# Optimization experiments

Measured on AMD Instinct MI355X. Metric: run time of the kernel, lower is better.

## Reference

```python
import jax, jax.numpy as jnp
import numpy as np

B, NA, NL, D = 512, 128, 512, 128
KA, KL = 16, 16  # active_agents, lane_tokens


def _layernorm(x, g, b, eps=1e-5):
    m = x.mean(-1, keepdims=True)
    v = ((x - m) ** 2).mean(-1, keepdims=True)
    return (x - m) / jnp.sqrt(v + eps) * g + b


def setup_inputs() -> dict:
    key = jax.random.key(0)
    ks = jax.random.split(key, 16)
    s = D ** -0.5
    inp = {
        "actor_feat": jax.random.normal(ks[0], (B, NA, D), jnp.float32),
        "lane_feat": jax.random.normal(ks[1], (B, NL, D), jnp.float32),
        "lane_centers": jax.random.normal(ks[2], (B, NL, 2), jnp.float32) * 50.0,
        "x_centers": jax.random.normal(ks[3], (B, NA, 2), jnp.float32) * 50.0,
        "spike_rate": jax.random.uniform(ks[4], (B, NA), jnp.float32),
        "actor_valid": jax.random.randint(ks[5], (B, NA), 0, 2).astype(bool),
        "lane_valid": jax.random.randint(ks[6], (B, NL), 0, 2).astype(bool),
        # MLP layer 0
        "W0a": jax.random.normal(ks[7], (D, D), jnp.float32) * s,
        "b0a": jnp.zeros((D,), jnp.float32),
        "W0b": jax.random.normal(ks[8], (D, D), jnp.float32) * s,
        "b0b": jnp.zeros((D,), jnp.float32),
        # MLP layer 1
        "W1a": jax.random.normal(ks[9], (D, D), jnp.float32) * s,
        "b1a": jnp.zeros((D,), jnp.float32),
        "W1b": jax.random.normal(ks[10], (D, D), jnp.float32) * s,
        "b1b": jnp.zeros((D,), jnp.float32),
        # shared LayerNorm
        "gamma": jnp.ones((D,), jnp.float32),
        "beta": jnp.zeros((D,), jnp.float32),
    }
    return inp


def reference(actor_feat, lane_feat, lane_centers, x_centers, spike_rate,
              actor_valid, lane_valid,
              W0a, b0a, W0b, b0b, W1a, b1a, W1b, b1b, gamma, beta):
    bsel = jnp.arange(B)[:, None]  # [B,1] batch index for fancy gather/scatter

    # masked top-k over spike_rate -> active agent indices [B,KA]
    masked = jnp.where(actor_valid, spike_rate, -jnp.inf)
    _, aidx = jax.lax.top_k(masked, KA)

    # lane selection: min distance from any active agent, k smallest
    ac = x_centers[bsel, aidx]                                # [B,KA,2]
    diff = ac[:, :, None, :] - lane_centers[:, None, :, :]    # [B,KA,NL,2]
    pair_dist = jnp.sqrt((diff ** 2).sum(-1))                 # cdist [B,KA,NL]
    lane_dist = pair_dist.min(axis=1)                         # [B,NL]
    lane_dist = jnp.where(lane_valid, lane_dist, jnp.inf)
    _, lidx = jax.lax.top_k(-lane_dist, KL)                   # k smallest

    # gather nodes and run residual MLP + LayerNorm stack
    nodes = jnp.concatenate([actor_feat[bsel, aidx], lane_feat[bsel, lidx]], axis=1)  # [B,KA+KL,D]
    for (Wa, ba, Wb, bb) in ((W0a, b0a, W0b, b0b), (W1a, b1a, W1b, b1b)):
        h = jax.nn.gelu(nodes @ Wa + ba, approximate=False) @ Wb + bb
        nodes = _layernorm(nodes + h, gamma, beta)

    # scatter updated nodes back into the full pools
    actor_out = actor_feat.at[bsel, aidx].set(nodes[:, :KA])
    lane_out = lane_feat.at[bsel, lidx].set(nodes[:, KA:])
    return actor_out, lane_out
```

## Files before the change

kernel.cpp:

```cpp
#include <hip/hip_runtime.h>
#include <math.h>

#define Bsz 512
#define NA  128
#define NL  512
#define Dd  128
#define KA  16
#define KL  16

#define NIDX  512
#define NCB   3584
#define ACT4  2097152
#define TOT4  10485760
#define CSTRIDE (NCB * 256)

__global__ __launch_bounds__(256) void idx_copy_kernel(
    const float* __restrict__ spike, const unsigned char* __restrict__ avalid,
    const float* __restrict__ xc, const float* __restrict__ lc,
    const unsigned char* __restrict__ lvalid,
    const float* __restrict__ actor_feat, const float* __restrict__ lane_feat,
    int* __restrict__ aidx, int* __restrict__ lidx,
    float* __restrict__ out0, float* __restrict__ out1) {
  const int tid = threadIdx.x;

  if (blockIdx.x >= NIDX) {
    const float4* __restrict__ srcA = (const float4*)actor_feat;
    const float4* __restrict__ srcL = (const float4*)lane_feat;
    float4* __restrict__ dstA = (float4*)out0;
    float4* __restrict__ dstL = (float4*)out1;
    const int gid = (blockIdx.x - NIDX) * 256 + tid;
#pragma unroll 1
    for (int base = gid; base < TOT4; base += 4 * CSTRIDE) {
      float4 v[4]; int pp[4];
#pragma unroll
      for (int u = 0; u < 4; ++u) {
        pp[u] = base + u * CSTRIDE;
        if (pp[u] < TOT4)
          v[u] = (pp[u] < ACT4) ? srcA[pp[u]] : srcL[pp[u] - ACT4];
      }
#pragma unroll
      for (int u = 0; u < 4; ++u) {
        if (pp[u] < TOT4) {
          if (pp[u] < ACT4) dstA[pp[u]] = v[u];
          else              dstL[pp[u] - ACT4] = v[u];
        }
      }
    }
    return;
  }

  const int b = blockIdx.x;

  __shared__ float s_ax[KA], s_ay[KA];
  __shared__ int   s_ai[KA];
  __shared__ float s_ld[NL];
  __shared__ float s_rv[4];
  __shared__ int   s_ri[4];
  __shared__ int   s_flag;

  if (tid == 0) s_flag = 0;
  __syncthreads();
  {
    int any = 0;
    for (int i = tid; i < 4096; i += 256)
      if ((i & 3) && avalid[i]) any = 1;
    if (any) atomicOr(&s_flag, 1);
  }
  __syncthreads();
  const int isbyte = s_flag;

#define VALID_AT(P, I) (isbyte ? (int)(P)[I] : ((const int*)(P))[I])

  if (tid < 64) {
    float v0 = VALID_AT(avalid, b * NA + tid)      ? spike[b * NA + tid]      : -INFINITY;
    float v1 = VALID_AT(avalid, b * NA + tid + 64) ? spike[b * NA + tid + 64] : -INFINITY;
    for (int it = 0; it < KA; ++it) {
      float bv = v0; int bi = tid;
      if (v1 > bv) { bv = v1; bi = tid + 64; }
      for (int off = 32; off; off >>= 1) {
        float ov = __shfl_xor(bv, off);
        int   oi = __shfl_xor(bi, off);
        if (ov > bv || (ov == bv && oi < bi)) { bv = ov; bi = oi; }
      }
      if (bi == tid)      v0 = -INFINITY;
      if (bi == tid + 64) v1 = -INFINITY;
      if (tid == 0) s_ai[it] = bi;
    }
  }
  __syncthreads();
  if (tid < KA) {
    int a = s_ai[tid];
    aidx[b * KA + tid] = a;
    s_ax[tid] = xc[(b * NA + a) * 2 + 0];
    s_ay[tid] = xc[(b * NA + a) * 2 + 1];
  }
  __syncthreads();

  for (int l = tid; l < NL; l += 256) {
    float lx = lc[(b * NL + l) * 2 + 0];
    float ly = lc[(b * NL + l) * 2 + 1];
    float best = INFINITY;
#pragma unroll
    for (int a = 0; a < KA; ++a) {
      float dx = s_ax[a] - lx, dy = s_ay[a] - ly;
      float d2 = __fadd_rn(__fmul_rn(dx, dx), __fmul_rn(dy, dy));
      best = fminf(best, d2);
    }
    best = sqrtf(best);
    s_ld[l] = VALID_AT(lvalid, b * NL + l) ? best : INFINITY;
  }
  __syncthreads();

  const int wid = tid >> 6, lane = tid & 63;
  for (int it = 0; it < KL; ++it) {
    float bv = s_ld[tid]; int bi = tid;
    float v2 = s_ld[tid + 256];
    if (v2 < bv) { bv = v2; bi = tid + 256; }
    for (int off = 32; off; off >>= 1) {
      float ov = __shfl_xor(bv, off);
      int   oi = __shfl_xor(bi, off);
      if (ov < bv || (ov == bv && oi < bi)) { bv = ov; bi = oi; }
    }
    if (lane == 0) { s_rv[wid] = bv; s_ri[wid] = bi; }
    __syncthreads();
    if (tid == 0) {
      float fbv = s_rv[0]; int fbi = s_ri[0];
      for (int w = 1; w < 4; ++w)
        if (s_rv[w] < fbv || (s_rv[w] == fbv && s_ri[w] < fbi)) { fbv = s_rv[w]; fbi = s_ri[w]; }
      lidx[b * KL + it] = fbi;
      s_ld[fbi] = INFINITY;
    }
    __syncthreads();
  }
#undef VALID_AT
}


#define STAGE_LOAD(W, h)                                              \
  { const float4* wg4 = (const float4*)((W) + (h) * 8192);            \
    R0 = wg4[tid]; R1 = wg4[512 + tid];                               \
    R2 = wg4[1024 + tid]; R3 = wg4[1536 + tid]; }

#define STAGE_WRITE()                                                 \
  { float4* swg4 = (float4*)s_w;                                      \
    swg4[tid] = R0; swg4[512 + tid] = R1;                             \
    swg4[1024 + tid] = R2; swg4[1536 + tid] = R3; }

#define FMA_HALF(h)                                                   \
  _Pragma("unroll 4")                                                 \
  for (int g = 0; g < 16; ++g) {                                      \
    const float* wr = s_w + g * 4 * Dd;                               \
    float w00 = wr[j0],        w10 = wr[j1];                          \
    float w01 = wr[Dd + j0],   w11 = wr[Dd + j1];                     \
    float w02 = wr[2*Dd + j0], w12 = wr[2*Dd + j1];                   \
    float w03 = wr[3*Dd + j0], w13 = wr[3*Dd + j1];                   \
    _Pragma("unroll")                                                 \
    for (int n = 0; n < 8; ++n) {                                     \
      float4 xv = ((const float4*)s_xu[n0 + n])[(h) * 16 + g];        \
      acc0[n] = fmaf(xv.x, w00, acc0[n]); acc1[n] = fmaf(xv.x, w10, acc1[n]); \
      acc0[n] = fmaf(xv.y, w01, acc0[n]); acc1[n] = fmaf(xv.y, w11, acc1[n]); \
      acc0[n] = fmaf(xv.z, w02, acc0[n]); acc1[n] = fmaf(xv.z, w12, acc1[n]); \
      acc0[n] = fmaf(xv.w, w03, acc0[n]); acc1[n] = fmaf(xv.w, w13, acc1[n]); \
    }                                                                 \
  }

#define MATVEC(W, Bv)                                                 \
  { const float bias0 = (Bv)[j0], bias1 = (Bv)[j1];                   \
    _Pragma("unroll")                                                 \
    for (int n = 0; n < 8; ++n) { acc0[n] = bias0; acc1[n] = bias1; } \
    STAGE_LOAD(W, 0);                                                 \
    STAGE_WRITE(); __syncthreads();                                   \
    STAGE_LOAD(W, 1);                                                 \
    FMA_HALF(0);                                                      \
    __syncthreads();                                                  \
    STAGE_WRITE(); __syncthreads();                                   \
    FMA_HALF(1);                                                      \
    __syncthreads(); }

__global__ __launch_bounds__(512, 2) void mlp_kernel(
    const float* __restrict__ actor_feat, const float* __restrict__ lane_feat,
    const int* __restrict__ aidx, const int* __restrict__ lidx,
    const float* __restrict__ W0a, const float* __restrict__ b0a,
    const float* __restrict__ W0b, const float* __restrict__ b0b,
    const float* __restrict__ W1a, const float* __restrict__ b1a,
    const float* __restrict__ W1b, const float* __restrict__ b1b,
    const float* __restrict__ gamma, const float* __restrict__ beta,
    float* __restrict__ out0, float* __restrict__ out1) {
  __shared__ float s_w[64 * Dd];
  __shared__ float s_xu[64][Dd];
  __shared__ int   s_src[64];

  const int tid = threadIdx.x;
  const int wave = tid >> 6, lane = tid & 63;
  const int b0 = blockIdx.x * 2;

  if (tid < 64) {
    int rr = tid, bidx = b0 + (rr >> 5), lr = rr & 31;
    s_src[rr] = (lr < 16) ? aidx[bidx * KA + lr] : lidx[bidx * KL + lr - 16];
  }
  __syncthreads();

  const int n0 = wave * 8;
#pragma unroll
  for (int i = 0; i < 4; ++i) {
    int q = lane + 64 * i;
    int rr = n0 + (q >> 5), c4 = q & 31;
    int bidx = b0 + (rr >> 5), lr = rr & 31;
    const float* src = (lr < 16)
        ? actor_feat + ((size_t)bidx * NA + s_src[rr]) * Dd
        : lane_feat  + ((size_t)bidx * NL + s_src[rr]) * Dd;
    ((float4*)s_xu[rr])[c4] = ((const float4*)src)[c4];
  }

  const int j0 = lane, j1 = lane + 64;
  const float g0 = gamma[j0], g1 = gamma[j1];
  const float bt0 = beta[j0], bt1 = beta[j1];

  float acc0[8], acc1[8], rx0[8], rx1[8];
  float4 R0, R1, R2, R3;

#pragma unroll
  for (int n = 0; n < 8; ++n) {
    rx0[n] = s_xu[n0 + n][j0];
    rx1[n] = s_xu[n0 + n][j1];
  }

#pragma unroll 1
  for (int layer = 0; layer < 2; ++layer) {
    const float* wa = layer ? W1a : W0a;
    const float* ba = layer ? b1a : b0a;
    const float* wb = layer ? W1b : W0b;
    const float* bb = layer ? b1b : b0b;

    MATVEC(wa, ba);

#pragma unroll
    for (int n = 0; n < 8; ++n) {
      float t0 = acc0[n], t1 = acc1[n];
      s_xu[n0 + n][j0] = 0.5f * t0 * (1.0f + erff(t0 * 0.70710678118654752f));
      s_xu[n0 + n][j1] = 0.5f * t1 * (1.0f + erff(t1 * 0.70710678118654752f));
    }

    MATVEC(wb, bb);

#pragma unroll
    for (int n = 0; n < 8; ++n) {
      float r0 = rx0[n] + acc0[n];
      float r1 = rx1[n] + acc1[n];
      float sum = r0 + r1;
      for (int off = 32; off; off >>= 1) sum += __shfl_xor(sum, off);
      float mean = sum * (1.0f / 128.0f);
      float d0 = r0 - mean, d1 = r1 - mean;
      float sq = d0 * d0 + d1 * d1;
      for (int off = 32; off; off >>= 1) sq += __shfl_xor(sq, off);
      float inv = 1.0f / sqrtf(sq * (1.0f / 128.0f) + 1e-5f);
      float v0 = d0 * inv * g0 + bt0;
      float v1 = d1 * inv * g1 + bt1;
      if (layer == 0) {
        s_xu[n0 + n][j0] = v0; s_xu[n0 + n][j1] = v1;
        rx0[n] = v0; rx1[n] = v1;
      } else {
        int rr = n0 + n, bidx = b0 + (rr >> 5), lr = rr & 31, si = s_src[rr];
        float* dst = (lr < 16) ? out0 + ((size_t)bidx * NA + si) * Dd
                               : out1 + ((size_t)bidx * NL + si) * Dd;
        dst[j0] = v0;
        dst[j1] = v1;
      }
    }
  }
}

extern "C" void kernel_launch(void* const* d_in, const int* in_sizes, int n_in,
                              void* d_out, int out_size, void* d_ws, size_t ws_size,
                              hipStream_t stream) {
  const float* actor_feat = (const float*)d_in[0];
  const float* lane_feat  = (const float*)d_in[1];
  const float* lc         = (const float*)d_in[2];
  const float* xc         = (const float*)d_in[3];
  const float* spike      = (const float*)d_in[4];
  const unsigned char* avalid = (const unsigned char*)d_in[5];
  const unsigned char* lvalid = (const unsigned char*)d_in[6];
  const float* W0a = (const float*)d_in[7];
  const float* b0a = (const float*)d_in[8];
  const float* W0b = (const float*)d_in[9];
  const float* b0b = (const float*)d_in[10];
  const float* W1a = (const float*)d_in[11];
  const float* b1a = (const float*)d_in[12];
  const float* W1b = (const float*)d_in[13];
  const float* b1b = (const float*)d_in[14];
  const float* gamma = (const float*)d_in[15];
  const float* beta  = (const float*)d_in[16];

  int* aidx = (int*)d_ws;
  int* lidx = aidx + Bsz * KA;

  float* out0 = (float*)d_out;
  float* out1 = out0 + (size_t)Bsz * NA * Dd;

  idx_copy_kernel<<<NIDX + NCB, 256, 0, stream>>>(
      spike, avalid, xc, lc, lvalid, actor_feat, lane_feat,
      aidx, lidx, out0, out1);
  mlp_kernel<<<Bsz / 2, 512, 0, stream>>>(
      actor_feat, lane_feat, aidx, lidx,
      W0a, b0a, W0b, b0b, W1a, b1a, W1b, b1b, gamma, beta, out0, out1);
}
```

Baseline: 141.0 us.

## Replace fused copy blocks with hipMemcpyAsync and use float2 column pairs in MLP

Result: slower. 157.3 us (+11.5%).

```diff
diff --git a/kernel.cpp b/kernel.cpp
--- a/kernel.cpp
+++ b/kernel.cpp
@@ -8,48 +8,13 @@
 #define KA  16
 #define KL  16
 
-#define NIDX  512
-#define NCB   3584
-#define ACT4  2097152
-#define TOT4  10485760
-#define CSTRIDE (NCB * 256)
-
-__global__ __launch_bounds__(256) void idx_copy_kernel(
+__global__ __launch_bounds__(256) void idx_kernel(
     const float* __restrict__ spike, const unsigned char* __restrict__ avalid,
     const float* __restrict__ xc, const float* __restrict__ lc,
     const unsigned char* __restrict__ lvalid,
-    const float* __restrict__ actor_feat, const float* __restrict__ lane_feat,
-    int* __restrict__ aidx, int* __restrict__ lidx,
-    float* __restrict__ out0, float* __restrict__ out1) {
+    int* __restrict__ aidx, int* __restrict__ lidx) {
+  const int b = blockIdx.x;
   const int tid = threadIdx.x;
-
-  if (blockIdx.x >= NIDX) {
-    const float4* __restrict__ srcA = (const float4*)actor_feat;
-    const float4* __restrict__ srcL = (const float4*)lane_feat;
-    float4* __restrict__ dstA = (float4*)out0;
-    float4* __restrict__ dstL = (float4*)out1;
-    const int gid = (blockIdx.x - NIDX) * 256 + tid;
-#pragma unroll 1
-    for (int base = gid; base < TOT4; base += 4 * CSTRIDE) {
-      float4 v[4]; int pp[4];
-#pragma unroll
-      for (int u = 0; u < 4; ++u) {
-        pp[u] = base + u * CSTRIDE;
-        if (pp[u] < TOT4)
-          v[u] = (pp[u] < ACT4) ? srcA[pp[u]] : srcL[pp[u] - ACT4];
-      }
-#pragma unroll
-      for (int u = 0; u < 4; ++u) {
-        if (pp[u] < TOT4) {
-          if (pp[u] < ACT4) dstA[pp[u]] = v[u];
-          else              dstL[pp[u] - ACT4] = v[u];
-        }
-      }
-    }
-    return;
-  }
-
-  const int b = blockIdx.x;
 
   __shared__ float s_ax[KA], s_ay[KA];
   __shared__ int   s_ai[KA];
@@ -150,24 +115,24 @@
   _Pragma("unroll 4")                                                 \
   for (int g = 0; g < 16; ++g) {                                      \
     const float* wr = s_w + g * 4 * Dd;                               \
-    float w00 = wr[j0],        w10 = wr[j1];                          \
-    float w01 = wr[Dd + j0],   w11 = wr[Dd + j1];                     \
-    float w02 = wr[2*Dd + j0], w12 = wr[2*Dd + j1];                   \
-    float w03 = wr[3*Dd + j0], w13 = wr[3*Dd + j1];                   \
+    float2 w0 = *(const float2*)(wr + j0);                            \
+    float2 w1 = *(const float2*)(wr + Dd + j0);                       \
+    float2 w2 = *(const float2*)(wr + 2 * Dd + j0);                   \
+    float2 w3 = *(const float2*)(wr + 3 * Dd + j0);                   \
     _Pragma("unroll")                                                 \
     for (int n = 0; n < 8; ++n) {                                     \
       float4 xv = ((const float4*)s_xu[n0 + n])[(h) * 16 + g];        \
-      acc0[n] = fmaf(xv.x, w00, acc0[n]); acc1[n] = fmaf(xv.x, w10, acc1[n]); \
-      acc0[n] = fmaf(xv.y, w01, acc0[n]); acc1[n] = fmaf(xv.y, w11, acc1[n]); \
-      acc0[n] = fmaf(xv.z, w02, acc0[n]); acc1[n] = fmaf(xv.z, w12, acc1[n]); \
-      acc0[n] = fmaf(xv.w, w03, acc0[n]); acc1[n] = fmaf(xv.w, w13, acc1[n]); \
+      acc0[n] = fmaf(xv.x, w0.x, acc0[n]); acc1[n] = fmaf(xv.x, w0.y, acc1[n]); \
+      acc0[n] = fmaf(xv.y, w1.x, acc0[n]); acc1[n] = fmaf(xv.y, w1.y, acc1[n]); \
+      acc0[n] = fmaf(xv.z, w2.x, acc0[n]); acc1[n] = fmaf(xv.z, w2.y, acc1[n]); \
+      acc0[n] = fmaf(xv.w, w3.x, acc0[n]); acc1[n] = fmaf(xv.w, w3.y, acc1[n]); \
     }                                                                 \
   }
 
 #define MATVEC(W, Bv)                                                 \
-  { const float bias0 = (Bv)[j0], bias1 = (Bv)[j1];                   \
+  { const float2 bias = *(const float2*)((Bv) + j0);                  \
     _Pragma("unroll")                                                 \
-    for (int n = 0; n < 8; ++n) { acc0[n] = bias0; acc1[n] = bias1; } \
+    for (int n = 0; n < 8; ++n) { acc0[n] = bias.x; acc1[n] = bias.y; } \
     STAGE_LOAD(W, 0);                                                 \
     STAGE_WRITE(); __syncthreads();                                   \
     STAGE_LOAD(W, 1);                                                 \
@@ -212,9 +177,9 @@
     ((float4*)s_xu[rr])[c4] = ((const float4*)src)[c4];
   }
 
-  const int j0 = lane, j1 = lane + 64;
-  const float g0 = gamma[j0], g1 = gamma[j1];
-  const float bt0 = beta[j0], bt1 = beta[j1];
+  const int j0 = 2 * lane;
+  const float2 gm = *(const float2*)(gamma + j0);
+  const float2 bt = *(const float2*)(beta + j0);
 
   float acc0[8], acc1[8], rx0[8], rx1[8];
   float4 R0, R1, R2, R3;
@@ -222,7 +187,7 @@
 #pragma unroll
   for (int n = 0; n < 8; ++n) {
     rx0[n] = s_xu[n0 + n][j0];
-    rx1[n] = s_xu[n0 + n][j1];
+    rx1[n] = s_xu[n0 + n][j0 + 1];
   }
 
 #pragma unroll 1
@@ -237,8 +202,8 @@
 #pragma unroll
     for (int n = 0; n < 8; ++n) {
       float t0 = acc0[n], t1 = acc1[n];
-      s_xu[n0 + n][j0] = 0.5f * t0 * (1.0f + erff(t0 * 0.70710678118654752f));
-      s_xu[n0 + n][j1] = 0.5f * t1 * (1.0f + erff(t1 * 0.70710678118654752f));
+      s_xu[n0 + n][j0]     = 0.5f * t0 * (1.0f + erff(t0 * 0.70710678118654752f));
+      s_xu[n0 + n][j0 + 1] = 0.5f * t1 * (1.0f + erff(t1 * 0.70710678118654752f));
     }
 
     MATVEC(wb, bb);
@@ -254,17 +219,17 @@
       float sq = d0 * d0 + d1 * d1;
       for (int off = 32; off; off >>= 1) sq += __shfl_xor(sq, off);
       float inv = 1.0f / sqrtf(sq * (1.0f / 128.0f) + 1e-5f);
-      float v0 = d0 * inv * g0 + bt0;
-      float v1 = d1 * inv * g1 + bt1;
+      float v0 = d0 * inv * gm.x + bt.x;
+      float v1 = d1 * inv * gm.y + bt.y;
       if (layer == 0) {
-        s_xu[n0 + n][j0] = v0; s_xu[n0 + n][j1] = v1;
+        s_xu[n0 + n][j0] = v0; s_xu[n0 + n][j0 + 1] = v1;
         rx0[n] = v0; rx1[n] = v1;
       } else {
         int rr = n0 + n, bidx = b0 + (rr >> 5), lr = rr & 31, si = s_src[rr];
         float* dst = (lr < 16) ? out0 + ((size_t)bidx * NA + si) * Dd
                                : out1 + ((size_t)bidx * NL + si) * Dd;
-        dst[j0] = v0;
-        dst[j1] = v1;
+        float2 v = {v0, v1};
+        *(float2*)(dst + j0) = v;
       }
     }
   }
@@ -297,9 +262,11 @@
   float* out0 = (float*)d_out;
   float* out1 = out0 + (size_t)Bsz * NA * Dd;
 
-  idx_copy_kernel<<<NIDX + NCB, 256, 0, stream>>>(
-      spike, avalid, xc, lc, lvalid, actor_feat, lane_feat,
-      aidx, lidx, out0, out1);
+  idx_kernel<<<Bsz, 256, 0, stream>>>(spike, avalid, xc, lc, lvalid, aidx, lidx);
+  hipMemcpyAsync(out0, actor_feat, (size_t)Bsz * NA * Dd * sizeof(float),
+                 hipMemcpyDeviceToDevice, stream);
+  hipMemcpyAsync(out1, lane_feat, (size_t)Bsz * NL * Dd * sizeof(float),
+                 hipMemcpyDeviceToDevice, stream);
   mlp_kernel<<<Bsz / 2, 512, 0, stream>>>(
       actor_feat, lane_feat, aidx, lidx,
       W0a, b0a, W0b, b0b, W1a, b1a, W1b, b1b, gamma, beta, out0, out1);
```
